# Kernel optimization log

Measured on AMD Instinct MI355X. Metric: run time of the kernel, lower is better.

## Reference

```python
import jax, jax.numpy as jnp
from jax import lax
import numpy as np

I_CNN = 2048   # box feature dim
Q_H = 1024     # LSTM hidden
Q_E = 300      # word embedding dim
HID = 512      # gated MLP hidden
B = 256
MAXN = 100
T = 14


def setup_inputs() -> dict:
    key = jax.random.key(0)
    ks = jax.random.split(key, 12)
    w = lambda k, shape: (jax.random.normal(k, shape, dtype=jnp.float32) * 0.02)
    return {
        "wholefeat": jax.random.normal(ks[0], (B, I_CNN), dtype=jnp.float32),
        "pooled": jax.random.normal(ks[1], (B, I_CNN), dtype=jnp.float32),
        "box_feats": jax.random.normal(ks[2], (B, MAXN, I_CNN), dtype=jnp.float32),
        "q_feats": jax.random.normal(ks[3], (B, T, Q_E), dtype=jnp.float32),
        "box_coords": jax.random.uniform(ks[4], (B, MAXN, 4), dtype=jnp.float32),
        "index": jax.random.randint(ks[5], (B,), 1, MAXN + 1),
        # LSTM params (PyTorch layout: gates ordered i,f,g,o)
        "W_ih": w(ks[6], (4 * Q_H, Q_E)),
        "W_hh": w(ks[7], (4 * Q_H, Q_H)),
        "b_ih": jnp.zeros((4 * Q_H,), jnp.float32),
        "b_hh": jnp.zeros((4 * Q_H,), jnp.float32),
        # gated MLP params
        "W_w": w(ks[8], (HID, I_CNN + Q_H)),
        "W_b": jnp.zeros((HID,), jnp.float32),
        "Wp_w": w(ks[9], (HID, I_CNN + Q_H)),
        "Wp_b": jnp.zeros((HID,), jnp.float32),
        "f_w": w(ks[10], (1, HID)),
    }


def _lstm_last(x_tbe, W_ih, W_hh, b_ih, b_hh):
    # x_tbe: [T, B, E] time-major. Returns final hidden state h_T: [B, H].
    H = W_hh.shape[1]
    # precompute input projections for all timesteps: [T, B, 4H]
    xg = jnp.einsum('tbe,ge->tbg', x_tbe, W_ih) + (b_ih + b_hh)

    def step(carry, xt):
        h, c = carry
        gates = xt + h @ W_hh.T                       # [B, 4H]
        i, f, g, o = jnp.split(gates, 4, axis=-1)
        i = jax.nn.sigmoid(i)
        f = jax.nn.sigmoid(f)
        g = jnp.tanh(g)
        o = jax.nn.sigmoid(o)
        c = f * c + i * g
        h = o * jnp.tanh(c)
        return (h, c), None

    h0 = jnp.zeros((x_tbe.shape[1], H), x_tbe.dtype)
    (h, _), _ = lax.scan(step, (h0, h0), xg)
    return h


def reference(wholefeat, pooled, box_feats, q_feats, box_coords, index,
              W_ih, W_hh, b_ih, b_hh, W_w, W_b, Wp_w, Wp_b, f_w):
    # question encoding: last LSTM output per sample -> [B, Q_H]
    q_rnn = _lstm_last(jnp.transpose(q_feats, (1, 0, 2)), W_ih, W_hh, b_ih, b_hh)

    Bn, N, _ = box_feats.shape
    qst = jnp.broadcast_to(q_rnn[:, None, :], (Bn, N, q_rnn.shape[-1]))
    b_full = jnp.concatenate([box_feats, qst], axis=-1)        # [B, N, 3072]

    y_tilde = jnp.tanh(jnp.einsum('bnd,hd->bnh', b_full, W_w) + W_b)
    g = jax.nn.sigmoid(jnp.einsum('bnd,hd->bnh', b_full, Wp_w) + Wp_b)
    si = y_tilde * g                                           # [B, N, HID]
    wsi = jax.nn.sigmoid(jnp.einsum('bnh,oh->bno', si, f_w))[..., 0]  # [B, N]

    # ragged reduction: only the first index[i] boxes of sample i contribute
    mask = (jnp.arange(N)[None, :] < index[:, None]).astype(wsi.dtype)
    return jnp.sum(wsi * mask, axis=1)                         # [B]
```

## Files before the change

### kernel.cpp

```cpp
#include <hip/hip_runtime.h>
#include <cstdint>
#include <cstddef>

#define DEVI __device__ __forceinline__

typedef __attribute__((ext_vector_type(8))) short short8;
typedef __attribute__((ext_vector_type(4))) float f32x4;
typedef __attribute__((ext_vector_type(4))) int i32x4;
typedef __bf16 bf16x8 __attribute__((ext_vector_type(8)));

DEVI float sigf(float x) { return 1.0f / (1.0f + __expf(-x)); }
DEVI float tanh_f(float x) { return 2.0f / (1.0f + __expf(-2.0f * x)) - 1.0f; }

DEVI short f2bf(float x) {
    uint32_t u = __builtin_bit_cast(uint32_t, x);
    u += 0x7FFFu + ((u >> 16) & 1u);
    return (short)(u >> 16);
}
DEVI float bf2f(short s) {
    uint32_t u = ((uint32_t)(unsigned short)s) << 16;
    return __builtin_bit_cast(float, u);
}
DEVI uint32_t cvtpk(float lo, float hi) {
    uint32_t r;
    asm("v_cvt_pk_bf16_f32 %0, %1, %2" : "=v"(r) : "v"(lo), "v"(hi));
    return r;
}

DEVI void gload16(const void* g, void* l) {
    __builtin_amdgcn_global_load_lds(
        (const __attribute__((address_space(1))) void*)g,
        (__attribute__((address_space(3))) void*)l, 16, 0, 0);
}

DEVI f32x4 mfma16(short8 a, short8 b, f32x4 c) {
    return __builtin_amdgcn_mfma_f32_16x16x32_bf16(
        __builtin_bit_cast(bf16x8, a), __builtin_bit_cast(bf16x8, b), c, 0, 0, 0);
}


__global__ __launch_bounds__(256) void prep_wstk(const float* __restrict__ Wih,
                                                 const float* __restrict__ Whh,
                                                 const float* __restrict__ bih,
                                                 const float* __restrict__ bhh,
                                                 short* __restrict__ Wstk) {
    int idx = blockIdx.x * 256 + threadIdx.x;
    if (idx >= 4096 * 1344) return;
    int n = idx / 1344, k = idx - n * 1344;
    int hblk = n >> 6, gate = (n >> 4) & 3, hl = n & 15;
    int on = gate * 1024 + hblk * 16 + hl;
    float v = 0.f;
    if (k < 300) v = Wih[on * 300 + k];
    else if (k == 300) v = bih[on] + bhh[on];
    else if (k >= 320) v = Whh[on * 1024 + (k - 320)];
    Wstk[idx] = f2bf(v);
}

__global__ __launch_bounds__(256) void prep_x(const float* __restrict__ q,
                                              short* __restrict__ xb) {
    int idx = blockIdx.x * 256 + threadIdx.x;
    if (idx >= 14 * 256 * 320) return;
    int t = idx / (256 * 320);
    int r = idx - t * 256 * 320;
    int b = r / 320, e = r - b * 320;
    float v = (e < 300) ? q[(b * 14 + t) * 300 + e] : (e == 300 ? 1.0f : 0.0f);
    xb[idx] = f2bf(v);
}

__global__ __launch_bounds__(256) void prep_wcat(const float* __restrict__ Ww,
                                                 const float* __restrict__ Wpw,
                                                 short* __restrict__ Wcat) {
    int idx = blockIdx.x * 256 + threadIdx.x;
    if (idx >= 1024 * 3072) return;
    int n = idx / 3072, k = idx - n * 3072;
    int hg = n >> 5, which = (n >> 4) & 1, hl = n & 15;
    int h = hg * 16 + hl;
    const float* src = which ? Wpw : Ww;
    Wcat[idx] = f2bf(src[h * 3072 + k]);
}

__global__ __launch_bounds__(256) void prep_index(const int* __restrict__ index,
                                                  int* __restrict__ cum,
                                                  int* __restrict__ rowmap,
                                                  int* __restrict__ bmap) {
    __shared__ int s[256];
    int t = threadIdx.x;
    int myidx = index[t];
    s[t] = myidx;
    __syncthreads();
    for (int off = 1; off < 256; off <<= 1) {
        int v = (t >= off) ? s[t - off] : 0;
        __syncthreads();
        s[t] += v;
        __syncthreads();
    }
    cum[t + 1] = s[t];
    if (t == 0) cum[0] = 0;
    int base = s[t] - myidx;
    for (int j = 0; j < myidx; ++j) {
        rowmap[base + j] = t * 100 + j;
        bmap[base + j] = t;
    }
    int Ml = s[255];
    if (t < 128) { rowmap[Ml + t] = 0; bmap[Ml + t] = 0; }
}


__global__ __launch_bounds__(256) void xg_gemm(const short* __restrict__ xb,
                                               const short* __restrict__ Wstk,
                                               short* __restrict__ xg) {
    __shared__ __attribute__((aligned(16))) short As[128 * 64];
    __shared__ __attribute__((aligned(16))) short Bs[128 * 64];
    const int tid = threadIdx.x, l = tid & 63, w = tid >> 6;
    const int n0 = blockIdx.x * 128;
    const int m0 = blockIdx.y * 128;
    const int wm = w >> 1, wn = w & 1;

    const short* asrc[4];
    const short* bsrc[4];
    for (int i = 0; i < 4; i++) {
        int r = w * 32 + i * 8 + (l >> 3);
        int cs = (l & 7) ^ (r & 7);
        asrc[i] = xb + (size_t)(m0 + r) * 320 + cs * 8;
        bsrc[i] = Wstk + (size_t)(n0 + r) * 1344 + cs * 8;
    }

    f32x4 acc[4][4];
    for (int i = 0; i < 4; i++)
        for (int j = 0; j < 4; j++) acc[i][j] = f32x4{0.f, 0.f, 0.f, 0.f};

    for (int kt = 0; kt < 5; ++kt) {
        const int k0 = kt * 64;
        __syncthreads();
        for (int i = 0; i < 4; i++)
            gload16(asrc[i] + k0, &As[(w * 32 + i * 8) * 64]);
        for (int i = 0; i < 4; i++)
            gload16(bsrc[i] + k0, &Bs[(w * 32 + i * 8) * 64]);
        __syncthreads();
        for (int ks = 0; ks < 2; ++ks) {
            short8 a[4], b[4];
            for (int mf = 0; mf < 4; ++mf) {
                int m = wm * 64 + mf * 16 + (l & 15);
                int ca = (ks * 4 + (l >> 4)) ^ (m & 7);
                a[mf] = *(const short8*)&As[m * 64 + ca * 8];
            }
            for (int nf = 0; nf < 4; ++nf) {
                int n = wn * 64 + nf * 16 + (l & 15);
                int cb = (ks * 4 + (l >> 4)) ^ (n & 7);
                b[nf] = *(const short8*)&Bs[n * 64 + cb * 8];
            }
            for (int mf = 0; mf < 4; ++mf)
                for (int nf = 0; nf < 4; ++nf)
                    acc[mf][nf] = mfma16(a[mf], b[nf], acc[mf][nf]);
        }
    }
    const int hl = l & 15, hi = l >> 4;
    for (int mf = 0; mf < 4; ++mf)
        for (int nf = 0; nf < 4; ++nf)
            for (int rg = 0; rg < 4; ++rg) {
                int row = m0 + wm * 64 + mf * 16 + hi * 4 + rg;
                int col = n0 + wn * 64 + nf * 16 + hl;
                xg[(size_t)row * 4096 + col] = f2bf(acc[mf][nf][rg]);
            }
}


__global__ __launch_bounds__(128) void lstm_step(const short* __restrict__ hin,
                                                 const short* __restrict__ Wstk,
                                                 const short* __restrict__ xg_t,
                                                 float* __restrict__ c,
                                                 short* __restrict__ hout,
                                                 int dogemm) {
    __shared__ __attribute__((aligned(16))) short As[2][32 * 128];
    __shared__ __attribute__((aligned(16))) short Bs[2][64 * 128];
    const int tid = threadIdx.x, l = tid & 63, w = tid >> 6;
    const int hi = l >> 4, hl = l & 15;
    const int bid = blockIdx.x;
    const int xcd = bid & 7, ii = bid >> 3;
    const int ny = xcd * 8 + (ii & 7);
    const int mx = ii >> 3;
    const int m0 = mx * 32, n0g = ny * 64;

    f32x4 acc[4];
    for (int i = 0; i < 4; i++) acc[i] = f32x4{0.f, 0.f, 0.f, 0.f};

    if (dogemm) {
        const short* asrc[4];
        const short* bsrc[8];
        for (int i = 0; i < 4; i++) {
            int s = i * 128 + tid;
            int r = s >> 4, cs = s & 15;
            asrc[i] = hin + (size_t)(m0 + r) * 1024 + ((cs ^ (r & 15)) * 8);
        }
        for (int i = 0; i < 8; i++) {
            int s = i * 128 + tid;
            int r = s >> 4, cs = s & 15;
            bsrc[i] = Wstk + (size_t)(n0g + r) * 1344 + 320 + ((cs ^ (r & 15)) * 8);
        }
        for (int i = 0; i < 4; i++) gload16(asrc[i], &As[0][(i * 128 + tid) * 8]);
        for (int i = 0; i < 8; i++) gload16(bsrc[i], &Bs[0][(i * 128 + tid) * 8]);

        for (int kt = 0; kt < 8; ++kt) {
            const int cur = kt & 1;
            if (kt < 7) {
                const int k0 = (kt + 1) * 128;
                for (int i = 0; i < 4; i++)
                    gload16(asrc[i] + k0, &As[cur ^ 1][(i * 128 + tid) * 8]);
                for (int i = 0; i < 8; i++)
                    gload16(bsrc[i] + k0, &Bs[cur ^ 1][(i * 128 + tid) * 8]);
                asm volatile("s_waitcnt vmcnt(12)" ::: "memory");
            } else {
                asm volatile("s_waitcnt vmcnt(0)" ::: "memory");
            }
            __builtin_amdgcn_sched_barrier(0);
            __builtin_amdgcn_s_barrier();
            __builtin_amdgcn_sched_barrier(0);
#pragma unroll
            for (int ks = 0; ks < 4; ++ks) {
                const int mrow = w * 16 + hl;
                const int ca = (ks * 4 + hi) ^ hl;
                short8 a = *(const short8*)&As[cur][mrow * 128 + ca * 8];
#pragma unroll
                for (int nf = 0; nf < 4; ++nf) {
                    const int nrow = nf * 16 + hl;
                    short8 b = *(const short8*)&Bs[cur][nrow * 128 + ca * 8];
                    acc[nf] = mfma16(a, b, acc[nf]);
                }
            }
            __builtin_amdgcn_sched_barrier(0);
            asm volatile("s_waitcnt lgkmcnt(0)" ::: "memory");
            __builtin_amdgcn_s_barrier();
            __builtin_amdgcn_sched_barrier(0);
        }
    }

    const short* xr0 = xg_t + (size_t)(m0 + w * 16 + hi * 4) * 4096 + n0g + hl;
    for (int rg = 0; rg < 4; ++rg) {
        const short* xr = xr0 + (size_t)rg * 4096;
        float ig = acc[0][rg] + bf2f(xr[0]);
        float fg = acc[1][rg] + bf2f(xr[16]);
        float gg = acc[2][rg] + bf2f(xr[32]);
        float og = acc[3][rg] + bf2f(xr[48]);
        size_t off = (size_t)(m0 + w * 16 + hi * 4 + rg) * 1024 + ny * 16 + hl;
        float cn = sigf(fg) * c[off] + sigf(ig) * tanh_f(gg);
        c[off] = cn;
        hout[off] = f2bf(sigf(og) * tanh_f(cn));
    }
}


__global__ __launch_bounds__(256) void mlp_gemm(const float* __restrict__ box,
                                                const short* __restrict__ hb,
                                                const short* __restrict__ Wcat,
                                                const int* __restrict__ mliveptr,
                                                const int* __restrict__ rowmap,
                                                const int* __restrict__ bmap,
                                                const float* __restrict__ Wb,
                                                const float* __restrict__ Wpb,
                                                const float* __restrict__ fw,
                                                float* __restrict__ logits) {
    __shared__ __attribute__((aligned(16))) short As[128 * 64];
    __shared__ __attribute__((aligned(16))) short Bs[128 * 64];
    const int Mlive = *mliveptr;
    const int tid = threadIdx.x, l = tid & 63, w = tid >> 6;
    const int bid = blockIdx.x;
    const int xcd = bid & 7, ii = bid >> 3;
    const int x = ii & 7, q = ii >> 3;
    const int y = q * 8 + xcd;
    const int n0 = x * 128, m0 = y * 128;
    if (m0 >= Mlive) return;
    const int wm = w >> 1, wn = w & 1;

    const float* boxp[4];
    short* awr[4];
    for (int i = 0; i < 4; i++) {
        int slot = tid + i * 256;
        int r = slot >> 3, cc = slot & 7;
        boxp[i] = box + (size_t)rowmap[m0 + r] * 2048 + cc * 8;
        awr[i] = &As[r * 64 + ((cc ^ (r & 7)) * 8)];
    }
    const short* hsrc[4];
    const short* bsrc[4];
    for (int i = 0; i < 4; i++) {
        int r = w * 32 + i * 8 + (l >> 3);
        int cs = (l & 7) ^ (r & 7);
        hsrc[i] = hb + (size_t)bmap[m0 + r] * 1024 + cs * 8;
        bsrc[i] = Wcat + (size_t)(n0 + r) * 3072 + cs * 8;
    }

    f32x4 acc[4][4];
    for (int i = 0; i < 4; i++)
        for (int j = 0; j < 4; j++) acc[i][j] = f32x4{0.f, 0.f, 0.f, 0.f};

    float4 pva[4], pvb[4];
    for (int i = 0; i < 4; i++) {
        pva[i] = *(const float4*)(boxp[i]);
        pvb[i] = *(const float4*)(boxp[i] + 4);
    }

    for (int kt = 0; kt < 48; ++kt) {
        const int k0 = kt * 64;
        __builtin_amdgcn_sched_barrier(0);
        __builtin_amdgcn_s_barrier();
        __builtin_amdgcn_sched_barrier(0);
        if (kt < 32) {
            for (int i = 0; i < 4; i++) {
                i32x4 d;
                d[0] = (int)cvtpk(pva[i].x, pva[i].y);
                d[1] = (int)cvtpk(pva[i].z, pva[i].w);
                d[2] = (int)cvtpk(pvb[i].x, pvb[i].y);
                d[3] = (int)cvtpk(pvb[i].z, pvb[i].w);
                *(i32x4*)awr[i] = d;
            }
        } else {
            const int kq = k0 - 2048;
            for (int i = 0; i < 4; i++)
                gload16(hsrc[i] + kq, &As[(w * 32 + i * 8) * 64]);
        }
        for (int i = 0; i < 4; i++)
            gload16(bsrc[i] + k0, &Bs[(w * 32 + i * 8) * 64]);
        if (kt + 1 < 32) {
            const int k1 = (kt + 1) * 64;
            for (int i = 0; i < 4; i++) {
                pva[i] = *(const float4*)(boxp[i] + k1);
                pvb[i] = *(const float4*)(boxp[i] + k1 + 4);
            }
            asm volatile("s_waitcnt vmcnt(8) lgkmcnt(0)" ::: "memory");
        } else {
            asm volatile("s_waitcnt vmcnt(0) lgkmcnt(0)" ::: "memory");
        }
        __builtin_amdgcn_sched_barrier(0);
        __builtin_amdgcn_s_barrier();
        __builtin_amdgcn_sched_barrier(0);
        for (int ks = 0; ks < 2; ++ks) {
            short8 a[4], b[4];
            for (int mf = 0; mf < 4; ++mf) {
                int m = wm * 64 + mf * 16 + (l & 15);
                int ca = (ks * 4 + (l >> 4)) ^ (m & 7);
                a[mf] = *(const short8*)&As[m * 64 + ca * 8];
            }
            for (int nf = 0; nf < 4; ++nf) {
                int n = wn * 64 + nf * 16 + (l & 15);
                int cb = (ks * 4 + (l >> 4)) ^ (n & 7);
                b[nf] = *(const short8*)&Bs[n * 64 + cb * 8];
            }
            for (int mf = 0; mf < 4; ++mf)
                for (int nf = 0; nf < 4; ++nf)
                    acc[mf][nf] = mfma16(a[mf], b[nf], acc[mf][nf]);
        }
    }

    const int hl = l & 15, hi = l >> 4;
    for (int mf = 0; mf < 4; ++mf) {
        float part[4] = {0.f, 0.f, 0.f, 0.f};
        for (int p = 0; p < 2; ++p) {
            int ntg = (n0 + wn * 64) / 16 + 2 * p;
            int hg = ntg >> 1;
            int h = hg * 16 + hl;
            float fwv = fw[h], wbv = Wb[h], wpbv = Wpb[h];
            for (int rg = 0; rg < 4; ++rg) {
                float y2 = tanh_f(acc[mf][2 * p][rg] + wbv);
                float g2 = sigf(acc[mf][2 * p + 1][rg] + wpbv);
                part[rg] += y2 * g2 * fwv;
            }
        }
        for (int rg = 0; rg < 4; ++rg) {
            float v = part[rg];
            v += __shfl_xor(v, 1, 64);
            v += __shfl_xor(v, 2, 64);
            v += __shfl_xor(v, 4, 64);
            v += __shfl_xor(v, 8, 64);
            if (hl == 0) {
                int row = m0 + wm * 64 + mf * 16 + hi * 4 + rg;
                atomicAdd(&logits[row], v);
            }
        }
    }
}

__global__ __launch_bounds__(128) void reduce_out(const float* __restrict__ logits,
                                                  const int* __restrict__ index,
                                                  const int* __restrict__ cum,
                                                  float* __restrict__ out) {
    int b = blockIdx.x, t = threadIdx.x;
    int idx = index[b];
    int base = cum[b];
    float v = 0.f;
    if (t < 100 && t < idx) v = sigf(logits[base + t]);
    for (int m = 32; m; m >>= 1) v += __shfl_down(v, m, 64);
    __shared__ float s[2];
    if ((t & 63) == 0) s[t >> 6] = v;
    __syncthreads();
    if (t == 0) out[b] = s[0] + s[1];
}


extern "C" void kernel_launch(void* const* d_in, const int* in_sizes, int n_in,
                              void* d_out, int out_size, void* d_ws, size_t ws_size,
                              hipStream_t stream) {
    (void)in_sizes; (void)n_in; (void)out_size; (void)ws_size;
    const float* box = (const float*)d_in[2];
    const float* qf  = (const float*)d_in[3];
    const int* index = (const int*)d_in[5];
    const float* Wih = (const float*)d_in[6];
    const float* Whh = (const float*)d_in[7];
    const float* bih = (const float*)d_in[8];
    const float* bhh = (const float*)d_in[9];
    const float* Ww  = (const float*)d_in[10];
    const float* Wb  = (const float*)d_in[11];
    const float* Wpw = (const float*)d_in[12];
    const float* Wpb = (const float*)d_in[13];
    const float* fw  = (const float*)d_in[14];

    char* p = (char*)d_ws;
    short* Wstk = (short*)p;  p += (size_t)4096 * 1344 * 2;
    short* Wcat = (short*)p;  p += (size_t)1024 * 3072 * 2;
    short* xb   = (short*)p;  p += (size_t)3584 * 320 * 2;
    short* hb0  = (short*)p;  p += (size_t)256 * 1024 * 2;
    short* hb1  = (short*)p;  p += (size_t)256 * 1024 * 2;
    short* xg   = (short*)p;  p += (size_t)3584 * 4096 * 2;
    float* c    = (float*)p;  p += (size_t)256 * 1024 * 4;
    int*   cum  = (int*)p;    p += 260 * 4;
    int*   rowmap = (int*)p;  p += (size_t)(25600 + 128) * 4;
    int*   bmap = (int*)p;    p += (size_t)(25600 + 128) * 4;
    float* lgt  = (float*)p;  p += (size_t)25600 * 4;

    hipMemsetAsync(hb0, 0, (size_t)256 * 1024 * 2, stream);
    hipMemsetAsync(c, 0, (size_t)256 * 1024 * 4, stream);
    hipMemsetAsync(lgt, 0, (size_t)25600 * 4, stream);

    prep_index<<<1, 256, 0, stream>>>(index, cum, rowmap, bmap);
    prep_wstk<<<(4096 * 1344) / 256, 256, 0, stream>>>(Wih, Whh, bih, bhh, Wstk);
    prep_x<<<(14 * 256 * 320) / 256, 256, 0, stream>>>(qf, xb);
    prep_wcat<<<(1024 * 3072) / 256, 256, 0, stream>>>(Ww, Wpw, Wcat);

    xg_gemm<<<dim3(32, 28), 256, 0, stream>>>(xb, Wstk, xg);

    short* hbuf[2] = {hb0, hb1};
    for (int t = 0; t < 14; ++t) {
        lstm_step<<<512, 128, 0, stream>>>(
            hbuf[t & 1], Wstk, xg + (size_t)t * 256 * 4096, c,
            hbuf[(t & 1) ^ 1], t == 0 ? 0 : 1);
    }

    mlp_gemm<<<1600, 256, 0, stream>>>(box, hb0, Wcat, cum + 256, rowmap, bmap,
                                       Wb, Wpb, fw, lgt);
    reduce_out<<<256, 128, 0, stream>>>(lgt, index, cum, (float*)d_out);
}
```

Measured before the change: 346.7 us.

## Precompact live box rows to bf16 and load GEMM A tiles via LDS DMA

A new compact_box kernel converts only the live box rows to bf16 and packs them densely in a workspace buffer. mlp_gemm then fills its A tiles with direct global-to-LDS loads, the same way it loads the weights. This removes the per-tile fp32 register prefetch and conversion, and the indirect rowmap gather. The cost is an extra pass that writes a large bf16 intermediate and re-reads it, and the GEMM loop loses its register-prefetch overlap, falling back to plain syncthreads.

```diff
diff --git a/kernel.cpp b/kernel.cpp
--- a/kernel.cpp
+++ b/kernel.cpp
@@ -6,7 +6,6 @@
 
 typedef __attribute__((ext_vector_type(8))) short short8;
 typedef __attribute__((ext_vector_type(4))) float f32x4;
-typedef __attribute__((ext_vector_type(4))) int i32x4;
 typedef __bf16 bf16x8 __attribute__((ext_vector_type(8)));
 
 DEVI float sigf(float x) { return 1.0f / (1.0f + __expf(-x)); }
@@ -20,11 +19,6 @@
 DEVI float bf2f(short s) {
     uint32_t u = ((uint32_t)(unsigned short)s) << 16;
     return __builtin_bit_cast(float, u);
-}
-DEVI uint32_t cvtpk(float lo, float hi) {
-    uint32_t r;
-    asm("v_cvt_pk_bf16_f32 %0, %1, %2" : "=v"(r) : "v"(lo), "v"(hi));
-    return r;
 }
 
 DEVI void gload16(const void* g, void* l) {
@@ -105,6 +99,24 @@
     if (t < 128) { rowmap[Ml + t] = 0; bmap[Ml + t] = 0; }
 }
 
+__global__ __launch_bounds__(256) void compact_box(const float* __restrict__ box,
+                                                   const int* __restrict__ index,
+                                                   const int* __restrict__ cum,
+                                                   short* __restrict__ Ac) {
+    int m = blockIdx.x;
+    int b = m / 100, j = m - b * 100;
+    if (j >= index[b]) return;
+    size_t dr = (size_t)(cum[b] + j);
+    int t = threadIdx.x;
+    const float* src = box + (size_t)m * 2048 + t * 8;
+    float4 v0 = *(const float4*)src;
+    float4 v1 = *(const float4*)(src + 4);
+    short8 s;
+    s[0] = f2bf(v0.x); s[1] = f2bf(v0.y); s[2] = f2bf(v0.z); s[3] = f2bf(v0.w);
+    s[4] = f2bf(v1.x); s[5] = f2bf(v1.y); s[6] = f2bf(v1.z); s[7] = f2bf(v1.w);
+    *(short8*)&Ac[dr * 2048 + t * 8] = s;
+}
+
 
 __global__ __launch_bounds__(256) void xg_gemm(const short* __restrict__ xb,
                                                const short* __restrict__ Wstk,
@@ -249,11 +261,10 @@
 }
 
 
-__global__ __launch_bounds__(256) void mlp_gemm(const float* __restrict__ box,
+__global__ __launch_bounds__(256) void mlp_gemm(const short* __restrict__ Ac,
                                                 const short* __restrict__ hb,
                                                 const short* __restrict__ Wcat,
                                                 const int* __restrict__ mliveptr,
-                                                const int* __restrict__ rowmap,
                                                 const int* __restrict__ bmap,
                                                 const float* __restrict__ Wb,
                                                 const float* __restrict__ Wpb,
@@ -271,19 +282,13 @@
     if (m0 >= Mlive) return;
     const int wm = w >> 1, wn = w & 1;
 
-    const float* boxp[4];
-    short* awr[4];
-    for (int i = 0; i < 4; i++) {
-        int slot = tid + i * 256;
-        int r = slot >> 3, cc = slot & 7;
-        boxp[i] = box + (size_t)rowmap[m0 + r] * 2048 + cc * 8;
-        awr[i] = &As[r * 64 + ((cc ^ (r & 7)) * 8)];
-    }
+    const short* asrc[4];
     const short* hsrc[4];
     const short* bsrc[4];
     for (int i = 0; i < 4; i++) {
         int r = w * 32 + i * 8 + (l >> 3);
         int cs = (l & 7) ^ (r & 7);
+        asrc[i] = Ac + (size_t)(m0 + r) * 2048 + cs * 8;
         hsrc[i] = hb + (size_t)bmap[m0 + r] * 1024 + cs * 8;
         bsrc[i] = Wcat + (size_t)(n0 + r) * 3072 + cs * 8;
     }
@@ -292,26 +297,12 @@
     for (int i = 0; i < 4; i++)
         for (int j = 0; j < 4; j++) acc[i][j] = f32x4{0.f, 0.f, 0.f, 0.f};
 
-    float4 pva[4], pvb[4];
-    for (int i = 0; i < 4; i++) {
-        pva[i] = *(const float4*)(boxp[i]);
-        pvb[i] = *(const float4*)(boxp[i] + 4);
-    }
-
     for (int kt = 0; kt < 48; ++kt) {
         const int k0 = kt * 64;
-        __builtin_amdgcn_sched_barrier(0);
-        __builtin_amdgcn_s_barrier();
-        __builtin_amdgcn_sched_barrier(0);
+        __syncthreads();
         if (kt < 32) {
-            for (int i = 0; i < 4; i++) {
-                i32x4 d;
-                d[0] = (int)cvtpk(pva[i].x, pva[i].y);
-                d[1] = (int)cvtpk(pva[i].z, pva[i].w);
-                d[2] = (int)cvtpk(pvb[i].x, pvb[i].y);
-                d[3] = (int)cvtpk(pvb[i].z, pvb[i].w);
-                *(i32x4*)awr[i] = d;
-            }
+            for (int i = 0; i < 4; i++)
+                gload16(asrc[i] + k0, &As[(w * 32 + i * 8) * 64]);
         } else {
             const int kq = k0 - 2048;
             for (int i = 0; i < 4; i++)
@@ -319,19 +310,7 @@
         }
         for (int i = 0; i < 4; i++)
             gload16(bsrc[i] + k0, &Bs[(w * 32 + i * 8) * 64]);
-        if (kt + 1 < 32) {
-            const int k1 = (kt + 1) * 64;
-            for (int i = 0; i < 4; i++) {
-                pva[i] = *(const float4*)(boxp[i] + k1);
-                pvb[i] = *(const float4*)(boxp[i] + k1 + 4);
-            }
-            asm volatile("s_waitcnt vmcnt(8) lgkmcnt(0)" ::: "memory");
-        } else {
-            asm volatile("s_waitcnt vmcnt(0) lgkmcnt(0)" ::: "memory");
-        }
-        __builtin_amdgcn_sched_barrier(0);
-        __builtin_amdgcn_s_barrier();
-        __builtin_amdgcn_sched_barrier(0);
+        __syncthreads();
         for (int ks = 0; ks < 2; ++ks) {
             short8 a[4], b[4];
             for (int mf = 0; mf < 4; ++mf) {
@@ -424,6 +403,8 @@
     int*   rowmap = (int*)p;  p += (size_t)(25600 + 128) * 4;
     int*   bmap = (int*)p;    p += (size_t)(25600 + 128) * 4;
     float* lgt  = (float*)p;  p += (size_t)25600 * 4;
+    p = (char*)(((uintptr_t)p + 255) & ~(uintptr_t)255);
+    short* Ac   = (short*)p;  p += (size_t)25600 * 2048 * 2;
 
     hipMemsetAsync(hb0, 0, (size_t)256 * 1024 * 2, stream);
     hipMemsetAsync(c, 0, (size_t)256 * 1024 * 4, stream);
@@ -433,6 +414,8 @@
     prep_wstk<<<(4096 * 1344) / 256, 256, 0, stream>>>(Wih, Whh, bih, bhh, Wstk);
     prep_x<<<(14 * 256 * 320) / 256, 256, 0, stream>>>(qf, xb);
     prep_wcat<<<(1024 * 3072) / 256, 256, 0, stream>>>(Ww, Wpw, Wcat);
+
+    compact_box<<<25600, 256, 0, stream>>>(box, index, cum, Ac);
 
     xg_gemm<<<dim3(32, 28), 256, 0, stream>>>(xb, Wstk, xg);
 
@@ -443,7 +426,7 @@
             hbuf[(t & 1) ^ 1], t == 0 ? 0 : 1);
     }
 
-    mlp_gemm<<<1600, 256, 0, stream>>>(box, hb0, Wcat, cum + 256, rowmap, bmap,
+    mlp_gemm<<<1600, 256, 0, stream>>>(Ac, hb0, Wcat, cum + 256, bmap,
                                        Wb, Wpb, fw, lgt);
     reduce_out<<<256, 128, 0, stream>>>(lgt, index, cum, (float*)d_out);
 }
```

After: 351.7 us. No clear change (+1.4%).
